# Kernel tuning notes

Measured on AMD Instinct MI355X. Metric: run time of the kernel, lower is better.

The kernel has to match this reference:

```python
import jax, jax.numpy as jnp
import numpy as np

B, T, E, H, V = 64, 32, 512, 512, 32000


def setup_inputs() -> dict:
    key = jax.random.key(0)
    ks = jax.random.split(key, 9)
    s = 0.05
    return {
        "features": jax.random.normal(ks[0], (B, E), jnp.float32),
        "captions": jax.random.randint(ks[1], (B, T), 0, V),
        "seq_len": T,
        "embed_table": jax.random.normal(ks[2], (V, E), jnp.float32) * s,
        "W_ih": jax.random.normal(ks[3], (4 * H, E), jnp.float32) * s,
        "W_hh": jax.random.normal(ks[4], (4 * H, H), jnp.float32) * s,
        "b_ih": jax.random.normal(ks[5], (4 * H,), jnp.float32) * s,
        "b_hh": jax.random.normal(ks[6], (4 * H,), jnp.float32) * s,
        "W_out": jax.random.normal(ks[7], (V, H), jnp.float32) * s,
        "b_out": jax.random.normal(ks[8], (V,), jnp.float32) * s,
    }


def _lstm_cell(x, h, c, W_ih, W_hh, b_ih, b_hh):
    # gates: (B, 4H), PyTorch LSTMCell gate order i, f, g, o
    gates = x @ W_ih.T + b_ih + h @ W_hh.T + b_hh
    i, f, g, o = jnp.split(gates, 4, axis=-1)
    c_new = jax.nn.sigmoid(f) * c + jax.nn.sigmoid(i) * jnp.tanh(g)
    h_new = jax.nn.sigmoid(o) * jnp.tanh(c_new)
    return h_new, c_new


def reference(features, captions, seq_len, embed_table, W_ih, W_hh, b_ih, b_hh, W_out, b_out):
    batch = features.shape[0]
    hdim = W_hh.shape[1]
    h0 = jnp.zeros((batch, hdim), features.dtype)
    c0 = jnp.zeros((batch, hdim), features.dtype)
    # prime the state with image features
    h, c = _lstm_cell(features, h0, c0, W_ih, W_hh, b_ih, b_hh)

    cap_emb = embed_table[captions]          # (B, T, E)
    xs = jnp.swapaxes(cap_emb, 0, 1)         # (T, B, E) for scan

    def step(carry, x_t):
        h, c = carry
        h, c = _lstm_cell(x_t, h, c, W_ih, W_hh, b_ih, b_hh)
        # dropout is identity in eval mode
        out = h @ W_out.T + b_out             # (B, V)
        return (h, c), out

    _, outs = jax.lax.scan(step, (h, c), xs)  # (T, B, V)
    return jnp.swapaxes(outs, 0, 1)           # (B, T, V)
```

## Files before the change

### kernel.cpp

```cpp
#include <hip/hip_runtime.h>
#include <stdint.h>

#define BB 64
#define TT 32
#define EE 512
#define HH 512
#define VV 32000
#define G4 2048

typedef _Float16 f16x8 __attribute__((ext_vector_type(8)));
typedef float f32x4 __attribute__((ext_vector_type(4)));

__device__ __forceinline__ unsigned short f2h(float f) {
  return __builtin_bit_cast(unsigned short, (_Float16)f);
}
__device__ __forceinline__ void gload_lds16(const unsigned short* g, unsigned short* l) {
  __builtin_amdgcn_global_load_lds((const __attribute__((address_space(1))) void*)g,
                                   (__attribute__((address_space(3))) void*)l, 16, 0, 0);
}
__device__ __forceinline__ float sigm(float x) { return 1.f / (1.f + __expf(-x)); }
__device__ __forceinline__ float tanh_fast(float x) {
  return 1.f - 2.f / (__expf(2.f * x) + 1.f);
}

__global__ __launch_bounds__(256) void k_gemm_ih(const float* __restrict__ feat,
                                                 const int* __restrict__ cap,
                                                 const float* __restrict__ emb,
                                                 const float* __restrict__ Bw,
                                                 const float* __restrict__ bih,
                                                 const float* __restrict__ bhh,
                                                 float* __restrict__ C) {
  __shared__ float As[16][128];
  __shared__ float Bs[16][128];
  const int tid = threadIdx.x;
  const int bx = blockIdx.x & 15;
  const int by = blockIdx.x >> 4;
  const int m0 = by * 128, n0 = bx * 128;
  const int tx = tid & 15, ty = tid >> 4;

  float acc[8][8];
#pragma unroll
  for (int i = 0; i < 8; i++)
#pragma unroll
    for (int j = 0; j < 8; j++) acc[i][j] = 0.f;

  const int lr = tid >> 1;
  const int lk = (tid & 1) * 8;
  int arow = m0 + lr; if (arow > 2111) arow = 2111;
  const float* Ap;
  if (arow < BB) {
    Ap = feat + (size_t)arow * EE + lk;
  } else {
    int idx = arow - BB;
    int t = idx >> 6, b = idx & 63;
    Ap = emb + (size_t)cap[b * TT + t] * EE + lk;
  }
  const int brow = n0 + lr;
  const float* Bp = Bw + (size_t)brow * EE + lk;

  for (int k0 = 0; k0 < EE; k0 += 16) {
    float4 a0 = *(const float4*)(Ap + k0);
    float4 a1 = *(const float4*)(Ap + k0 + 4);
    float4 b0 = *(const float4*)(Bp + k0);
    float4 b1 = *(const float4*)(Bp + k0 + 4);
    __syncthreads();
    As[lk + 0][lr] = a0.x; As[lk + 1][lr] = a0.y; As[lk + 2][lr] = a0.z; As[lk + 3][lr] = a0.w;
    As[lk + 4][lr] = a1.x; As[lk + 5][lr] = a1.y; As[lk + 6][lr] = a1.z; As[lk + 7][lr] = a1.w;
    Bs[lk + 0][lr] = b0.x; Bs[lk + 1][lr] = b0.y; Bs[lk + 2][lr] = b0.z; Bs[lk + 3][lr] = b0.w;
    Bs[lk + 4][lr] = b1.x; Bs[lk + 5][lr] = b1.y; Bs[lk + 6][lr] = b1.z; Bs[lk + 7][lr] = b1.w;
    __syncthreads();
#pragma unroll
    for (int k = 0; k < 16; k++) {
      float a[8], b[8];
      *(float4*)&a[0] = *(const float4*)&As[k][ty * 8];
      *(float4*)&a[4] = *(const float4*)&As[k][ty * 8 + 4];
      *(float4*)&b[0] = *(const float4*)&Bs[k][tx * 8];
      *(float4*)&b[4] = *(const float4*)&Bs[k][tx * 8 + 4];
#pragma unroll
      for (int i = 0; i < 8; i++)
#pragma unroll
        for (int j = 0; j < 8; j++) acc[i][j] += a[i] * b[j];
    }
  }

  float bs[8];
#pragma unroll
  for (int j = 0; j < 8; j++) {
    int n = n0 + tx * 8 + j;
    bs[j] = bih[n] + bhh[n];
  }
#pragma unroll
  for (int i = 0; i < 8; i++) {
    int m = m0 + ty * 8 + i;
    if (m < 2112) {
      float4 o0, o1;
      o0.x = acc[i][0] + bs[0]; o0.y = acc[i][1] + bs[1];
      o0.z = acc[i][2] + bs[2]; o0.w = acc[i][3] + bs[3];
      o1.x = acc[i][4] + bs[4]; o1.y = acc[i][5] + bs[5];
      o1.z = acc[i][6] + bs[6]; o1.w = acc[i][7] + bs[7];
      *(float4*)(C + (size_t)m * G4 + n0 + tx * 8) = o0;
      *(float4*)(C + (size_t)m * G4 + n0 + tx * 8 + 4) = o1;
    }
  }
}

__device__ __forceinline__ void gridbar_nf(int* flags, int id) {
  asm volatile("s_waitcnt vmcnt(0)" ::: "memory");
  __syncthreads();
  if (threadIdx.x == 0)
    __hip_atomic_store(&flags[blockIdx.x], id, __ATOMIC_RELAXED, __HIP_MEMORY_SCOPE_AGENT);
  if (threadIdx.x < 64) {
    while (__hip_atomic_load(&flags[threadIdx.x], __ATOMIC_RELAXED, __HIP_MEMORY_SCOPE_AGENT) < id)
      __builtin_amdgcn_s_sleep(4);
  }
  __syncthreads();
}

__global__ __launch_bounds__(512) void k_rnn(const float* __restrict__ Gpre,
                                             const float* __restrict__ Whh,
                                             char* hseq_base,
                                             int* __restrict__ flags) {
  __shared__ __align__(16) unsigned short W_lds[32 * 512];
  __shared__ float gate_buf[2048];
  unsigned short* hseq16 = (unsigned short*)hseq_base;
  unsigned int* hseq32 = (unsigned int*)hseq_base;

  const int tid = threadIdx.x;
  const int bid = blockIdx.x;
  const int u0 = bid * 8;
  const int l = tid & 63;
  const int w = tid >> 6;
  const int lr = l & 15;
  const int kc = l >> 4;
  const int nt = w & 1;
  const int mt = w >> 1;
  const int es = w * 8 + (l >> 3);
  const int edu = l & 7;

  {
    int row = tid >> 4;
    int sub = tid & 15;
    int g = row >> 3, du = row & 7;
    const float* srcp = Whh + (size_t)(g * 512 + u0 + du) * HH;
#pragma unroll
    for (int c0 = 0; c0 < 4; ++c0) {
      int c = sub * 4 + c0;
      float4 va = *(const float4*)(srcp + c * 8);
      float4 vb = *(const float4*)(srcp + c * 8 + 4);
      __align__(16) unsigned short t8[8];
      t8[0] = f2h(va.x); t8[1] = f2h(va.y); t8[2] = f2h(va.z); t8[3] = f2h(va.w);
      t8[4] = f2h(vb.x); t8[5] = f2h(vb.y); t8[6] = f2h(vb.z); t8[7] = f2h(vb.w);
      *(int4*)((char*)W_lds + row * 1024 + ((c ^ (row & 7)) * 16)) = *(const int4*)t8;
    }
  }

  float c_reg;
  {
    const float* gp = Gpre + (size_t)es * G4 + u0 + edu;
    float gi = gp[0], gg = gp[1024], go = gp[1536];
    float cn = sigm(gi) * tanh_fast(gg);
    float hn = sigm(go) * tanh_fast(cn);
    c_reg = cn;
    unsigned int hb = f2h(hn);
    unsigned int other = (unsigned int)__shfl_xor((int)hb, 1);
    if (!(l & 1))
      __hip_atomic_store(&hseq32[(size_t)es * 256 + bid * 4 + (edu >> 1)],
                         hb | (other << 16), __ATOMIC_RELAXED, __HIP_MEMORY_SCOPE_AGENT);
  }

  float pre[4];
#pragma unroll
  for (int g = 0; g < 4; ++g)
    pre[g] = Gpre[((size_t)(1 * 64) + es) * G4 + g * 512 + u0 + edu];

  gridbar_nf(flags, 1);

  for (int s = 1; s <= TT; ++s) {
    const unsigned short* hin = hseq16 + (size_t)(s - 1) * BB * HH;

    f32x4 acc = {0.f, 0.f, 0.f, 0.f};
    const unsigned short* hbase = hin + (size_t)(mt * 16 + lr) * HH + kc * 8;
    const int wrow = nt * 16 + lr;
    const char* wbase = (const char*)W_lds + wrow * 1024;
#pragma unroll
    for (int kk = 0; kk < 16; ++kk) {
      uint4 hq = *(const uint4*)(hbase + kk * 32);
      int4 wq = *(const int4*)(wbase + (((kk * 4 + kc) ^ (wrow & 7)) * 16));
      f16x8 hf = __builtin_bit_cast(f16x8, hq);
      f16x8 wf = __builtin_bit_cast(f16x8, wq);
      acc = __builtin_amdgcn_mfma_f32_16x16x32_f16(hf, wf, acc, 0, 0, 0);
    }

    {
      int g = nt * 2 + (lr >> 3);
      int du = lr & 7;
#pragma unroll
      for (int j = 0; j < 4; ++j) {
        int ss = mt * 16 + kc * 4 + j;
        gate_buf[g * 512 + du * 64 + (ss ^ (du << 3))] = acc[j];
      }
    }
    __syncthreads();

    {
      float gi = gate_buf[0 * 512 + edu * 64 + (es ^ (edu << 3))] + pre[0];
      float gf = gate_buf[1 * 512 + edu * 64 + (es ^ (edu << 3))] + pre[1];
      float gg = gate_buf[2 * 512 + edu * 64 + (es ^ (edu << 3))] + pre[2];
      float go = gate_buf[3 * 512 + edu * 64 + (es ^ (edu << 3))] + pre[3];
      float cn = sigm(gf) * c_reg + sigm(gi) * tanh_fast(gg);
      float hn = sigm(go) * tanh_fast(cn);
      c_reg = cn;
      unsigned int hb = f2h(hn);
      unsigned int other = (unsigned int)__shfl_xor((int)hb, 1);
      if (!(l & 1))
        __hip_atomic_store(&hseq32[(size_t)s * 16384 + es * 256 + bid * 4 + (edu >> 1)],
                           hb | (other << 16), __ATOMIC_RELAXED, __HIP_MEMORY_SCOPE_AGENT);
    }

    if (s < TT) {
#pragma unroll
      for (int g = 0; g < 4; ++g)
        pre[g] = Gpre[((size_t)(s + 1) * 64 + es) * G4 + g * 512 + u0 + edu];
      gridbar_nf(flags, s + 1);
    }
  }
}

__global__ __launch_bounds__(512) void k_gemm_out(const unsigned short* __restrict__ hseq,
                                                  const float* __restrict__ Wout,
                                                  const float* __restrict__ bout,
                                                  float* __restrict__ out) {
  __shared__ __align__(16) unsigned short As[2][BB * HH];
  const int tid = threadIdx.x;
  const int l = tid & 63;
  const int w = tid >> 6;
  const int n00 = blockIdx.x * 128;
  const int bcol = w * 16 + (l >> 4) * 4;
  const float4 bo0 = *(const float4*)(bout + n00 + bcol);

  const int vr0 = n00 + w * 16 + (l & 15);
  const int kb = (l >> 4) * 8;
  uint4 w0r[16];
#pragma unroll
  for (int kt = 0; kt < 16; ++kt) {
    const float* p = Wout + (size_t)vr0 * HH + kt * 32 + kb;
    float4 a = *(const float4*)p;
    float4 b = *(const float4*)(p + 4);
    __align__(16) unsigned short t8[8];
    t8[0] = f2h(a.x); t8[1] = f2h(a.y); t8[2] = f2h(a.z); t8[3] = f2h(a.w);
    t8[4] = f2h(b.x); t8[5] = f2h(b.y); t8[6] = f2h(b.z); t8[7] = f2h(b.w);
    w0r[kt] = *(const uint4*)t8;
  }

  const unsigned short* hs1 = hseq + (size_t)1 * (BB * HH);
#pragma unroll
  for (int it = 0; it < 8; ++it) {
    int ci = it * 512 + tid;
    int row = ci >> 6, cd = ci & 63;
    gload_lds16(hs1 + (size_t)row * HH + (cd ^ (row & 7)) * 8, As[0] + ci * 8);
  }

  int cur = 0;
  for (int s = 1; s <= TT; ++s) {
    asm volatile("s_waitcnt vmcnt(0)" ::: "memory");
    __syncthreads();

    if (s < TT) {
      const unsigned short* hs = hseq + (size_t)(s + 1) * (BB * HH);
#pragma unroll
      for (int it = 0; it < 8; ++it) {
        int ci = it * 512 + tid;
        int row = ci >> 6, cd = ci & 63;
        gload_lds16(hs + (size_t)row * HH + (cd ^ (row & 7)) * 8, As[cur ^ 1] + ci * 8);
      }
    }

    const unsigned short* Ab = As[cur];
    f32x4 acc0[4];
#pragma unroll
    for (int m = 0; m < 4; ++m) acc0[m] = (f32x4){0.f, 0.f, 0.f, 0.f};
#pragma unroll
    for (int m = 0; m < 4; ++m) {
      int row = m * 16 + (l & 15);
#pragma unroll
      for (int kt = 0; kt < 16; ++kt) {
        int c = kt * 4 + (l >> 4);
        f16x8 af = *(const f16x8*)&Ab[row * HH + (c ^ (row & 7)) * 8];
        acc0[m] = __builtin_amdgcn_mfma_f32_16x16x32_f16(
            __builtin_bit_cast(f16x8, w0r[kt]), af, acc0[m], 0, 0, 0);
      }
    }
#pragma unroll
    for (int m = 0; m < 4; ++m) {
      int b = m * 16 + (l & 15);
      float* orow = out + ((size_t)(b * TT + (s - 1))) * VV + n00 + bcol;
      float4 v;
      v.x = acc0[m][0] + bo0.x;
      v.y = acc0[m][1] + bo0.y;
      v.z = acc0[m][2] + bo0.z;
      v.w = acc0[m][3] + bo0.w;
      *(float4*)orow = v;
    }
    cur ^= 1;
  }
}

extern "C" void kernel_launch(void* const* d_in, const int* in_sizes, int n_in,
                              void* d_out, int out_size, void* d_ws, size_t ws_size,
                              hipStream_t stream) {
  const float* feat = (const float*)d_in[0];
  const int* cap = (const int*)d_in[1];
  const float* emb = (const float*)d_in[3];
  const float* Wih = (const float*)d_in[4];
  const float* Whh = (const float*)d_in[5];
  const float* bih = (const float*)d_in[6];
  const float* bhh = (const float*)d_in[7];
  const float* Wout = (const float*)d_in[8];
  const float* bout = (const float*)d_in[9];
  float* out = (float*)d_out;

  char* ws = (char*)d_ws;
  float* Gpre = (float*)ws;
  char* hseq = ws + 17301504;
  int* flags = (int*)(ws + 19464192);

  hipMemsetAsync(flags, 0, 4096, stream);
  k_gemm_ih<<<dim3(17 * 16), dim3(256), 0, stream>>>(feat, cap, emb, Wih, bih, bhh, Gpre);
  k_rnn<<<dim3(64), dim3(512), 0, stream>>>(Gpre, Whh, hseq, flags);
  k_gemm_out<<<dim3(250), dim3(512), 0, stream>>>((const unsigned short*)hseq, Wout, bout, out);
}
```

Baseline: 460.8 us.

## Fuse input projection into persistent LSTM kernel with W_ih held in LDS

Removes the separate fp32 SIMT GEMM that precomputed the input-gate projections for all timesteps. Embeddings are now gathered and converted to fp16 by a light kernel, and the recurrent kernel keeps both W_ih and W_hh slices in LDS, computing x@W_ih with MFMA alongside h@W_hh at each step. This avoids the large Gpre write/read and the slow FMA GEMM, at the cost of doubling MFMA work inside the serial recurrent loop and larger LDS use per block.

```diff
diff --git a/kernel.cpp b/kernel.cpp
--- a/kernel.cpp
+++ b/kernel.cpp
@@ -23,85 +23,23 @@
   return 1.f - 2.f / (__expf(2.f * x) + 1.f);
 }
 
-__global__ __launch_bounds__(256) void k_gemm_ih(const float* __restrict__ feat,
-                                                 const int* __restrict__ cap,
-                                                 const float* __restrict__ emb,
-                                                 const float* __restrict__ Bw,
-                                                 const float* __restrict__ bih,
-                                                 const float* __restrict__ bhh,
-                                                 float* __restrict__ C) {
-  __shared__ float As[16][128];
-  __shared__ float Bs[16][128];
-  const int tid = threadIdx.x;
-  const int bx = blockIdx.x & 15;
-  const int by = blockIdx.x >> 4;
-  const int m0 = by * 128, n0 = bx * 128;
-  const int tx = tid & 15, ty = tid >> 4;
-
-  float acc[8][8];
-#pragma unroll
-  for (int i = 0; i < 8; i++)
-#pragma unroll
-    for (int j = 0; j < 8; j++) acc[i][j] = 0.f;
-
-  const int lr = tid >> 1;
-  const int lk = (tid & 1) * 8;
-  int arow = m0 + lr; if (arow > 2111) arow = 2111;
-  const float* Ap;
-  if (arow < BB) {
-    Ap = feat + (size_t)arow * EE + lk;
+__global__ __launch_bounds__(128) void k_embed(const float* __restrict__ feat,
+                                               const int* __restrict__ cap,
+                                               const float* __restrict__ emb,
+                                               unsigned short* __restrict__ xseq) {
+  const int r = blockIdx.x;
+  const int t = threadIdx.x;
+  const float* src;
+  if (r < BB) {
+    src = feat + (size_t)r * EE;
   } else {
-    int idx = arow - BB;
-    int t = idx >> 6, b = idx & 63;
-    Ap = emb + (size_t)cap[b * TT + t] * EE + lk;
-  }
-  const int brow = n0 + lr;
-  const float* Bp = Bw + (size_t)brow * EE + lk;
-
-  for (int k0 = 0; k0 < EE; k0 += 16) {
-    float4 a0 = *(const float4*)(Ap + k0);
-    float4 a1 = *(const float4*)(Ap + k0 + 4);
-    float4 b0 = *(const float4*)(Bp + k0);
-    float4 b1 = *(const float4*)(Bp + k0 + 4);
-    __syncthreads();
-    As[lk + 0][lr] = a0.x; As[lk + 1][lr] = a0.y; As[lk + 2][lr] = a0.z; As[lk + 3][lr] = a0.w;
-    As[lk + 4][lr] = a1.x; As[lk + 5][lr] = a1.y; As[lk + 6][lr] = a1.z; As[lk + 7][lr] = a1.w;
-    Bs[lk + 0][lr] = b0.x; Bs[lk + 1][lr] = b0.y; Bs[lk + 2][lr] = b0.z; Bs[lk + 3][lr] = b0.w;
-    Bs[lk + 4][lr] = b1.x; Bs[lk + 5][lr] = b1.y; Bs[lk + 6][lr] = b1.z; Bs[lk + 7][lr] = b1.w;
-    __syncthreads();
-#pragma unroll
-    for (int k = 0; k < 16; k++) {
-      float a[8], b[8];
-      *(float4*)&a[0] = *(const float4*)&As[k][ty * 8];
-      *(float4*)&a[4] = *(const float4*)&As[k][ty * 8 + 4];
-      *(float4*)&b[0] = *(const float4*)&Bs[k][tx * 8];
-      *(float4*)&b[4] = *(const float4*)&Bs[k][tx * 8 + 4];
-#pragma unroll
-      for (int i = 0; i < 8; i++)
-#pragma unroll
-        for (int j = 0; j < 8; j++) acc[i][j] += a[i] * b[j];
-    }
-  }
-
-  float bs[8];
-#pragma unroll
-  for (int j = 0; j < 8; j++) {
-    int n = n0 + tx * 8 + j;
-    bs[j] = bih[n] + bhh[n];
-  }
-#pragma unroll
-  for (int i = 0; i < 8; i++) {
-    int m = m0 + ty * 8 + i;
-    if (m < 2112) {
-      float4 o0, o1;
-      o0.x = acc[i][0] + bs[0]; o0.y = acc[i][1] + bs[1];
-      o0.z = acc[i][2] + bs[2]; o0.w = acc[i][3] + bs[3];
-      o1.x = acc[i][4] + bs[4]; o1.y = acc[i][5] + bs[5];
-      o1.z = acc[i][6] + bs[6]; o1.w = acc[i][7] + bs[7];
-      *(float4*)(C + (size_t)m * G4 + n0 + tx * 8) = o0;
-      *(float4*)(C + (size_t)m * G4 + n0 + tx * 8 + 4) = o1;
-    }
-  }
+    int p = r >> 6, b = r & 63;
+    src = emb + (size_t)cap[b * TT + (p - 1)] * EE;
+  }
+  float4 v = ((const float4*)src)[t];
+  ushort4 o;
+  o.x = f2h(v.x); o.y = f2h(v.y); o.z = f2h(v.z); o.w = f2h(v.w);
+  ((ushort4*)(xseq + (size_t)r * EE))[t] = o;
 }
 
 __device__ __forceinline__ void gridbar_nf(int* flags, int id) {
@@ -116,11 +54,14 @@
   __syncthreads();
 }
 
-__global__ __launch_bounds__(512) void k_rnn(const float* __restrict__ Gpre,
+__global__ __launch_bounds__(512) void k_rnn(const unsigned short* __restrict__ xseq,
+                                             const float* __restrict__ Wih,
                                              const float* __restrict__ Whh,
+                                             const float* __restrict__ bih,
+                                             const float* __restrict__ bhh,
                                              char* hseq_base,
                                              int* __restrict__ flags) {
-  __shared__ __align__(16) unsigned short W_lds[32 * 512];
+  __shared__ __align__(16) unsigned short W_lds[32 * 1024];
   __shared__ float gate_buf[2048];
   unsigned short* hseq16 = (unsigned short*)hseq_base;
   unsigned int* hseq32 = (unsigned int*)hseq_base;
@@ -136,61 +77,48 @@
   const int mt = w >> 1;
   const int es = w * 8 + (l >> 3);
   const int edu = l & 7;
+  const int wrow = nt * 16 + lr;
 
   {
     int row = tid >> 4;
     int sub = tid & 15;
     int g = row >> 3, du = row & 7;
-    const float* srcp = Whh + (size_t)(g * 512 + u0 + du) * HH;
-#pragma unroll
-    for (int c0 = 0; c0 < 4; ++c0) {
-      int c = sub * 4 + c0;
-      float4 va = *(const float4*)(srcp + c * 8);
-      float4 vb = *(const float4*)(srcp + c * 8 + 4);
+    const float* pih = Wih + (size_t)(g * 512 + u0 + du) * EE;
+    const float* phh = Whh + (size_t)(g * 512 + u0 + du) * HH;
+#pragma unroll
+    for (int c0 = 0; c0 < 8; ++c0) {
+      int c = sub * 8 + c0;
+      const float* src = (c < 64) ? (pih + c * 8) : (phh + (c - 64) * 8);
+      float4 va = *(const float4*)src;
+      float4 vb = *(const float4*)(src + 4);
       __align__(16) unsigned short t8[8];
       t8[0] = f2h(va.x); t8[1] = f2h(va.y); t8[2] = f2h(va.z); t8[3] = f2h(va.w);
       t8[4] = f2h(vb.x); t8[5] = f2h(vb.y); t8[6] = f2h(vb.z); t8[7] = f2h(vb.w);
-      *(int4*)((char*)W_lds + row * 1024 + ((c ^ (row & 7)) * 16)) = *(const int4*)t8;
-    }
-  }
+      *(int4*)&W_lds[row * 1024 + ((c ^ (row & 7)) * 8)] = *(const int4*)t8;
+    }
+  }
+
+  float bsum[4];
+#pragma unroll
+  for (int g = 0; g < 4; ++g) {
+    int n = g * 512 + u0 + edu;
+    bsum[g] = bih[n] + bhh[n];
+  }
+  __syncthreads();
+
+  const char* wbase = (const char*)W_lds + wrow * 2048;
 
   float c_reg;
   {
-    const float* gp = Gpre + (size_t)es * G4 + u0 + edu;
-    float gi = gp[0], gg = gp[1024], go = gp[1536];
-    float cn = sigm(gi) * tanh_fast(gg);
-    float hn = sigm(go) * tanh_fast(cn);
-    c_reg = cn;
-    unsigned int hb = f2h(hn);
-    unsigned int other = (unsigned int)__shfl_xor((int)hb, 1);
-    if (!(l & 1))
-      __hip_atomic_store(&hseq32[(size_t)es * 256 + bid * 4 + (edu >> 1)],
-                         hb | (other << 16), __ATOMIC_RELAXED, __HIP_MEMORY_SCOPE_AGENT);
-  }
-
-  float pre[4];
-#pragma unroll
-  for (int g = 0; g < 4; ++g)
-    pre[g] = Gpre[((size_t)(1 * 64) + es) * G4 + g * 512 + u0 + edu];
-
-  gridbar_nf(flags, 1);
-
-  for (int s = 1; s <= TT; ++s) {
-    const unsigned short* hin = hseq16 + (size_t)(s - 1) * BB * HH;
-
     f32x4 acc = {0.f, 0.f, 0.f, 0.f};
-    const unsigned short* hbase = hin + (size_t)(mt * 16 + lr) * HH + kc * 8;
-    const int wrow = nt * 16 + lr;
-    const char* wbase = (const char*)W_lds + wrow * 1024;
+    const unsigned short* xb = xseq + (size_t)(mt * 16 + lr) * EE + kc * 8;
 #pragma unroll
     for (int kk = 0; kk < 16; ++kk) {
-      uint4 hq = *(const uint4*)(hbase + kk * 32);
+      uint4 xq = *(const uint4*)(xb + kk * 32);
       int4 wq = *(const int4*)(wbase + (((kk * 4 + kc) ^ (wrow & 7)) * 16));
-      f16x8 hf = __builtin_bit_cast(f16x8, hq);
-      f16x8 wf = __builtin_bit_cast(f16x8, wq);
-      acc = __builtin_amdgcn_mfma_f32_16x16x32_f16(hf, wf, acc, 0, 0, 0);
-    }
-
+      acc = __builtin_amdgcn_mfma_f32_16x16x32_f16(
+          __builtin_bit_cast(f16x8, xq), __builtin_bit_cast(f16x8, wq), acc, 0, 0, 0);
+    }
     {
       int g = nt * 2 + (lr >> 3);
       int du = lr & 7;
@@ -201,12 +129,62 @@
       }
     }
     __syncthreads();
-
     {
-      float gi = gate_buf[0 * 512 + edu * 64 + (es ^ (edu << 3))] + pre[0];
-      float gf = gate_buf[1 * 512 + edu * 64 + (es ^ (edu << 3))] + pre[1];
-      float gg = gate_buf[2 * 512 + edu * 64 + (es ^ (edu << 3))] + pre[2];
-      float go = gate_buf[3 * 512 + edu * 64 + (es ^ (edu << 3))] + pre[3];
+      float gi = gate_buf[0 * 512 + edu * 64 + (es ^ (edu << 3))] + bsum[0];
+      float gg = gate_buf[2 * 512 + edu * 64 + (es ^ (edu << 3))] + bsum[2];
+      float go = gate_buf[3 * 512 + edu * 64 + (es ^ (edu << 3))] + bsum[3];
+      float cn = sigm(gi) * tanh_fast(gg);
+      float hn = sigm(go) * tanh_fast(cn);
+      c_reg = cn;
+      unsigned int hb = f2h(hn);
+      unsigned int other = (unsigned int)__shfl_xor((int)hb, 1);
+      if (!(l & 1))
+        __hip_atomic_store(&hseq32[(size_t)es * 256 + bid * 4 + (edu >> 1)],
+                           hb | (other << 16), __ATOMIC_RELAXED, __HIP_MEMORY_SCOPE_AGENT);
+    }
+  }
+  gridbar_nf(flags, 1);
+
+  for (int s = 1; s <= TT; ++s) {
+    const unsigned short* xb = xseq + (size_t)s * (BB * HH) + (size_t)(mt * 16 + lr) * EE + kc * 8;
+    const unsigned short* hb2 = hseq16 + (size_t)(s - 1) * (BB * HH) + (size_t)(mt * 16 + lr) * HH + kc * 8;
+
+    f32x4 acca = {0.f, 0.f, 0.f, 0.f};
+    f32x4 accb = {0.f, 0.f, 0.f, 0.f};
+#pragma unroll
+    for (int kk = 0; kk < 16; ++kk) {
+      uint4 xq = *(const uint4*)(xb + kk * 32);
+      int4 wq = *(const int4*)(wbase + (((kk * 4 + kc) ^ (wrow & 7)) * 16));
+      acca = __builtin_amdgcn_mfma_f32_16x16x32_f16(
+          __builtin_bit_cast(f16x8, xq), __builtin_bit_cast(f16x8, wq), acca, 0, 0, 0);
+    }
+#pragma unroll
+    for (int kk = 16; kk < 32; ++kk) {
+      uint4 hq = *(const uint4*)(hb2 + (kk - 16) * 32);
+      int4 wq = *(const int4*)(wbase + (((kk * 4 + kc) ^ (wrow & 7)) * 16));
+      accb = __builtin_amdgcn_mfma_f32_16x16x32_f16(
+          __builtin_bit_cast(f16x8, hq), __builtin_bit_cast(f16x8, wq), accb, 0, 0, 0);
+    }
+    f32x4 acc;
+#pragma unroll
+    for (int j = 0; j < 4; ++j) acc[j] = acca[j] + accb[j];
+
+    {
+      int g = nt * 2 + (lr >> 3);
+      int du = lr & 7;
+#pragma unroll
+      for (int j = 0; j < 4; ++j) {
+        int ss = mt * 16 + kc * 4 + j;
+        gate_buf[g * 512 + du * 64 + (ss ^ (du << 3))] = acc[j];
+      }
+    }
+    __syncthreads();
+
+    {
+      float gi = gate_buf[0 * 512 + edu * 64 + (es ^ (edu << 3))] + bsum[0];
+      float gf = gate_buf[1 * 512 + edu * 64 + (es ^ (edu << 3))] + bsum[1];
+      float gg = gate_buf[2 * 512 + edu * 64 + (es ^ (edu << 3))] + bsum[2];
+      float go = gate_buf[3 * 512 + edu * 64 + (es ^ (edu << 3))] + bsum[3];
       float cn = sigm(gf) * c_reg + sigm(gi) * tanh_fast(gg);
       float hn = sigm(go) * tanh_fast(cn);
       c_reg = cn;
@@ -217,12 +195,7 @@
                            hb | (other << 16), __ATOMIC_RELAXED, __HIP_MEMORY_SCOPE_AGENT);
     }
 
-    if (s < TT) {
-#pragma unroll
-      for (int g = 0; g < 4; ++g)
-        pre[g] = Gpre[((size_t)(s + 1) * 64 + es) * G4 + g * 512 + u0 + edu];
-      gridbar_nf(flags, s + 1);
-    }
+    if (s < TT) gridbar_nf(flags, s + 1);
   }
 }
 
@@ -320,12 +293,12 @@
   float* out = (float*)d_out;
 
   char* ws = (char*)d_ws;
-  float* Gpre = (float*)ws;
-  char* hseq = ws + 17301504;
-  int* flags = (int*)(ws + 19464192);
+  unsigned short* xseq = (unsigned short*)ws;
+  char* hseq = ws + 2162688;
+  int* flags = (int*)(ws + 4325376);
 
   hipMemsetAsync(flags, 0, 4096, stream);
-  k_gemm_ih<<<dim3(17 * 16), dim3(256), 0, stream>>>(feat, cap, emb, Wih, bih, bhh, Gpre);
-  k_rnn<<<dim3(64), dim3(512), 0, stream>>>(Gpre, Whh, hseq, flags);
+  k_embed<<<dim3(2112), dim3(128), 0, stream>>>(feat, cap, emb, xseq);
+  k_rnn<<<dim3(64), dim3(512), 0, stream>>>(xseq, Wih, Whh, bih, bhh, hseq, flags);
   k_gemm_out<<<dim3(250), dim3(512), 0, stream>>>((const unsigned short*)hseq, Wout, bout, out);
 }
```

Result: slower. 487.7 us (+5.8%).
